# Kernel optimization log

Hardware: AMD Instinct MI355X
Metric: run time of the kernel (lower is better)

## Reference

```python
import jax, jax.numpy as jnp
import numpy as np

B, C, W, H = 4, 128, 64, 64
CK = 32  # f/g projection channels


def setup_inputs() -> dict:
    key = jax.random.key(0)
    ks = jax.random.split(key, 8)
    s_in = 1.0 / np.sqrt(C)
    return {
        "x": jax.random.normal(ks[0], (B, C, W, H), dtype=jnp.float32),
        "Wf": jax.random.normal(ks[1], (CK, C), dtype=jnp.float32) * s_in,
        "bf": jnp.zeros((CK,), dtype=jnp.float32),
        "Wg": jax.random.normal(ks[2], (CK, C), dtype=jnp.float32) * s_in,
        "bg": jnp.zeros((CK,), dtype=jnp.float32),
        "Wh": jax.random.normal(ks[3], (C, C), dtype=jnp.float32) * s_in,
        "bh": jnp.zeros((C,), dtype=jnp.float32),
        "gamma": jax.random.normal(ks[4], (1,), dtype=jnp.float32) * 0.1,
    }


def reference(x, Wf, bf, Wg, bg, Wh, bh, gamma):
    b, c, w, h = x.shape
    n = w * h
    xf = x.reshape(b, c, n)                                  # [B,C,N]
    # 1x1 convs == per-pixel linear projections
    f = jnp.einsum('oc,bcn->bon', Wf, xf) + bf[None, :, None]  # [B,32,N]
    g = jnp.einsum('oc,bcn->bon', Wg, xf) + bg[None, :, None]  # [B,32,N]
    v = jnp.einsum('oc,bcn->bon', Wh, xf) + bh[None, :, None]  # [B,C,N]
    # attention = softmax(f^T g) over last dim (g positions), as in the torch code
    att = jax.nn.softmax(jnp.einsum('bkn,bkm->bnm', f, g), axis=-1)  # [B,N,N]
    # self_attention = h @ attention  (contract over f-position axis)
    sa = jnp.einsum('bcn,bnm->bcm', v, att).reshape(b, c, w, h)
    return gamma[0] * sa + x
```

## Files before the change

kernel.cpp:

```cpp
#include <hip/hip_runtime.h>
#include <hip/hip_bf16.h>

#define BB 4
#define CC 128
#define NN 4096
#define CK 32
#define L2E 1.442695040888963f

typedef __attribute__((ext_vector_type(8))) short short8v;
typedef __attribute__((ext_vector_type(4))) float float4v;

__device__ inline ushort f2bf(float f) {
    union { __hip_bfloat16 h; ushort u; } cv;
    cv.h = __float2bfloat16(f);
    return cv.u;
}
__device__ inline uint pk2(float lo, float hi) {
    return ((uint)f2bf(lo)) | ((uint)f2bf(hi) << 16);
}
__device__ __forceinline__ void gll16(const void* g, void* l) {
    __builtin_amdgcn_global_load_lds(
        (const __attribute__((address_space(1))) void*)g,
        (__attribute__((address_space(3))) void*)l, 16, 0, 0);
}
__device__ __forceinline__ void gll4(const void* g, void* l) {
    __builtin_amdgcn_global_load_lds(
        (const __attribute__((address_space(1))) void*)g,
        (__attribute__((address_space(3))) void*)l, 4, 0, 0);
}

__global__ __launch_bounds__(1024) void proj_kernel(
    const float* __restrict__ x,
    const float* __restrict__ Wf, const float* __restrict__ bf,
    const float* __restrict__ Wg, const float* __restrict__ bg,
    const float* __restrict__ Wh, const float* __restrict__ bh,
    const float* __restrict__ gamma,
    ushort* __restrict__ ft, ushort* __restrict__ gt, ushort* __restrict__ vh)
{
    __shared__ float xs[CC][64];
    const int t  = threadIdx.x;
    const int n0 = blockIdx.x * 64;
    const int b  = blockIdx.y;
    const float* xb = x + (size_t)b * CC * NN + n0;

    {
        const int j  = t & 63;
        const int cb = t >> 6;
        #pragma unroll
        for (int i = 0; i < 8; ++i)
            xs[cb + 16 * i][j] = xb[(size_t)(cb + 16 * i) * NN + j];
    }
    __syncthreads();

    const int jq = t & 15;
    const int og = (t >> 4) & 15;
    const int i3 = t >> 8;

    const float* wrow[3];
    float biasv[3];
    int   mode[3], oc[3];
    #pragma unroll
    for (int ii = 0; ii < 3; ++ii) {
        const int i = i3 * 3 + ii;
        if (i < 2)      { oc[ii] = og + 16 * i;       wrow[ii] = Wf + oc[ii] * CC; biasv[ii] = bf[oc[ii]]; mode[ii] = 0; }
        else if (i < 4) { oc[ii] = og + 16 * (i - 2); wrow[ii] = Wg + oc[ii] * CC; biasv[ii] = bg[oc[ii]]; mode[ii] = 1; }
        else            { oc[ii] = og + 16 * (i - 4); wrow[ii] = Wh + oc[ii] * CC; biasv[ii] = bh[oc[ii]]; mode[ii] = 2; }
    }

    float acc[3][4];
    #pragma unroll
    for (int ii = 0; ii < 3; ++ii)
        #pragma unroll
        for (int jj = 0; jj < 4; ++jj) acc[ii][jj] = 0.f;

    #pragma unroll 4
    for (int c4 = 0; c4 < 32; ++c4) {
        float4 wv[3];
        #pragma unroll
        for (int ii = 0; ii < 3; ++ii)
            wv[ii] = *reinterpret_cast<const float4*>(&wrow[ii][c4 * 4]);
        #pragma unroll
        for (int q = 0; q < 4; ++q) {
            const float4 xv = *reinterpret_cast<const float4*>(&xs[c4 * 4 + q][jq * 4]);
            #pragma unroll
            for (int ii = 0; ii < 3; ++ii) {
                const float wq = (q == 0) ? wv[ii].x : (q == 1) ? wv[ii].y
                               : (q == 2) ? wv[ii].z : wv[ii].w;
                acc[ii][0] += wq * xv.x;
                acc[ii][1] += wq * xv.y;
                acc[ii][2] += wq * xv.z;
                acc[ii][3] += wq * xv.w;
            }
        }
    }

    const float sgn = (gamma[0] < 0.f) ? -1.f : 1.f;
    const int n_base = n0 + jq * 4;
    #pragma unroll
    for (int ii = 0; ii < 3; ++ii) {
        if (mode[ii] == 0) {
            #pragma unroll
            for (int jj = 0; jj < 4; ++jj)
                ft[((size_t)b * NN + n_base + jj) * CK + oc[ii]] = f2bf(acc[ii][jj] + biasv[ii]);
        } else if (mode[ii] == 1) {
            #pragma unroll
            for (int jj = 0; jj < 4; ++jj)
                gt[((size_t)b * NN + n_base + jj) * CK + oc[ii]] = f2bf(acc[ii][jj] + biasv[ii]);
        } else {
            ushort4 pkv;
            pkv.x = f2bf(sgn * (acc[ii][0] + biasv[ii]));
            pkv.y = f2bf(sgn * (acc[ii][1] + biasv[ii]));
            pkv.z = f2bf(sgn * (acc[ii][2] + biasv[ii]));
            pkv.w = f2bf(sgn * (acc[ii][3] + biasv[ii]));
            *reinterpret_cast<ushort4*>(&vh[((size_t)b * CC + oc[ii]) * NN + n_base]) = pkv;
        }
    }
}

__global__ __launch_bounds__(256) void pass1_kernel(
    const ushort* __restrict__ ft, const ushort* __restrict__ gt,
    float* __restrict__ Dpart)
{
    const int t   = threadIdx.x;
    const int w   = t >> 6;
    const int l   = t & 63;
    const int g16 = l >> 4;
    const int l16 = l & 15;
    const int n0  = blockIdx.x * 64;
    const int b   = blockIdx.y;
    const int mz  = blockIdx.z;

    const ushort* ftb = ft + (size_t)b * NN * CK;
    const ushort* gtb = gt + (size_t)b * NN * CK;

    const short8v afrag = *reinterpret_cast<const short8v*>(
        &ftb[(size_t)(n0 + 16 * w + l16) * CK + 8 * g16]);

    const float4v zf = {0.f, 0.f, 0.f, 0.f};
    float d0 = 0.f, d1 = 0.f, d2 = 0.f, d3 = 0.f;
    const int m0 = mz * 512;

    short8v bfA = *reinterpret_cast<const short8v*>(
        &gtb[(size_t)(m0 + l16) * CK + 8 * g16]);
    #pragma unroll 1
    for (int mt = 0; mt < 32; mt += 2) {
        const short8v bfB = *reinterpret_cast<const short8v*>(
            &gtb[(size_t)(m0 + (mt + 1) * 16 + l16) * CK + 8 * g16]);
        float4v s = __builtin_amdgcn_mfma_f32_16x16x32_bf16(afrag, bfA, zf, 0, 0, 0);
        d0 += __expf(s[0]); d1 += __expf(s[1]); d2 += __expf(s[2]); d3 += __expf(s[3]);
        bfA = *reinterpret_cast<const short8v*>(
            &gtb[(size_t)(m0 + (((mt + 2) & 31)) * 16 + l16) * CK + 8 * g16]);
        float4v s2 = __builtin_amdgcn_mfma_f32_16x16x32_bf16(afrag, bfB, zf, 0, 0, 0);
        d0 += __expf(s2[0]); d1 += __expf(s2[1]); d2 += __expf(s2[2]); d3 += __expf(s2[3]);
    }
    #pragma unroll
    for (int msk = 1; msk <= 8; msk <<= 1) {
        d0 += __shfl_xor(d0, msk);
        d1 += __shfl_xor(d1, msk);
        d2 += __shfl_xor(d2, msk);
        d3 += __shfl_xor(d3, msk);
    }
    if (l16 < 4) {
        const int n = n0 + 16 * w + 4 * g16 + l16;
        const float v = (l16 == 0) ? d0 : (l16 == 1) ? d1 : (l16 == 2) ? d2 : d3;
        Dpart[((size_t)b * NN + n) * 8 + mz] = v;
    }
}

__global__ __launch_bounds__(256) void reduce_kernel(
    const float* __restrict__ Dpart, float* __restrict__ Ld,
    const float* __restrict__ gamma)
{
    const int i = blockIdx.x * 256 + threadIdx.x;
    const float4 a4 = *reinterpret_cast<const float4*>(&Dpart[(size_t)i * 8]);
    const float4 b4 = *reinterpret_cast<const float4*>(&Dpart[(size_t)i * 8 + 4]);
    const float D = (a4.x + a4.y + a4.z + a4.w) + (b4.x + b4.y + b4.z + b4.w);
    Ld[i] = log2f(fabsf(gamma[0])) - log2f(D);
}

#define V_OFF 0
#define F_OFF 4096
#define L_OFF 6144
#define BUFB  6400
#define WSTR  12800

__global__ __launch_bounds__(512) void pass2_kernel(
    const ushort* __restrict__ ft, const ushort* __restrict__ gt,
    const ushort* __restrict__ vh, const float* __restrict__ Ld,
    const float* __restrict__ x, float* __restrict__ out)
{
    __shared__ __align__(16) char smem[8 * WSTR];

    const int t   = threadIdx.x;
    const int w   = t >> 6;
    const int l   = t & 63;
    const int g16 = l >> 4;
    const int l16 = l & 15;
    const int ch  = w & 1;
    const int nq  = w >> 1;

    const int bid = blockIdx.x;
    const int xcd = bid & 7;
    const int b   = xcd >> 1;
    const int m0  = ((bid >> 3) + 32 * (xcd & 1)) * 64;

    const ushort* ftb = ft + (size_t)b * NN * CK;
    const ushort* gtb = gt + (size_t)b * NN * CK;
    const ushort* vhb = vh + (size_t)b * CC * NN;
    const float*  ldb = Ld + (size_t)b * NN;

    char* wsm = smem + w * WSTR;

    short8v gfrag[4];
    #pragma unroll
    for (int tm = 0; tm < 4; ++tm)
        gfrag[tm] = *reinterpret_cast<const short8v*>(
            &gtb[(size_t)(m0 + 16 * tm + l16) * CK + 8 * g16]);

    const float4v zf = {0.f, 0.f, 0.f, 0.f};
    float4v acc[4][4];
    #pragma unroll
    for (int tc = 0; tc < 4; ++tc)
        #pragma unroll
        for (int tm = 0; tm < 4; ++tm) acc[tc][tm] = zf;

    const int nbase = nq * 1024;
    const int rr = l >> 2, cp = l & 3;

#define STAGE(n0_, bo_) do {                                                   \
    _Pragma("unroll")                                                          \
    for (int j = 0; j < 4; ++j) {                                              \
        const int row = j * 16 + rr;                                           \
        gll16(vhb + (size_t)(64 * ch + row) * NN + (n0_)                       \
                  + (((2 * cp) ^ (row & 6)) << 2),                             \
              wsm + (bo_) + V_OFF + j * 1024);                                 \
    }                                                                          \
    _Pragma("unroll")                                                          \
    for (int j = 0; j < 2; ++j) {                                              \
        const int row = j * 16 + rr;                                           \
        gll16(ftb + (size_t)((n0_) + row) * CK + cp * 8,                       \
              wsm + (bo_) + F_OFF + j * 1024);                                 \
    }                                                                          \
    gll4(ldb + (n0_) + (l & 31), wsm + (bo_) + L_OFF);                         \
} while (0)

    STAGE(nbase, 0);
    asm volatile("s_waitcnt vmcnt(0)" ::: "memory");

    int bo = 0;
    #pragma unroll 1
    for (int st = 0; st < 32; ++st) {
        const int n0 = nbase + st * 32;
        if (st < 31) {
            STAGE(n0 + 32, bo ^ BUFB);
            asm volatile("s_waitcnt vmcnt(7)" ::: "memory");
        } else {
            asm volatile("s_waitcnt vmcnt(0)" ::: "memory");
        }

        const char*  Vb = wsm + bo + V_OFF;
        const char*  Fb = wsm + bo + F_OFF;
        const float* Lb = (const float*)(wsm + bo + L_OFF);

        const short8v af0 = *reinterpret_cast<const short8v*>(Fb + l16 * 64 + g16 * 16);
        const short8v af1 = *reinterpret_cast<const short8v*>(Fb + (16 + l16) * 64 + g16 * 16);
        const float4  ld0 = *reinterpret_cast<const float4*>(Lb + 4 * g16);
        const float4  ld1 = *reinterpret_cast<const float4*>(Lb + 16 + 4 * g16);

        union { uint u[4]; short8v s; } pf[4];
        #pragma unroll
        for (int tm = 0; tm < 4; ++tm) {
            float4v s0 = __builtin_amdgcn_mfma_f32_16x16x32_bf16(af0, gfrag[tm], zf, 0, 0, 0);
            float4v s1 = __builtin_amdgcn_mfma_f32_16x16x32_bf16(af1, gfrag[tm], zf, 0, 0, 0);
            pf[tm].u[0] = pk2(__builtin_amdgcn_exp2f(fmaf(s0[0], L2E, ld0.x)),
                              __builtin_amdgcn_exp2f(fmaf(s0[1], L2E, ld0.y)));
            pf[tm].u[1] = pk2(__builtin_amdgcn_exp2f(fmaf(s0[2], L2E, ld0.z)),
                              __builtin_amdgcn_exp2f(fmaf(s0[3], L2E, ld0.w)));
            pf[tm].u[2] = pk2(__builtin_amdgcn_exp2f(fmaf(s1[0], L2E, ld1.x)),
                              __builtin_amdgcn_exp2f(fmaf(s1[1], L2E, ld1.y)));
            pf[tm].u[3] = pk2(__builtin_amdgcn_exp2f(fmaf(s1[2], L2E, ld1.z)),
                              __builtin_amdgcn_exp2f(fmaf(s1[3], L2E, ld1.w)));
        }

        #pragma unroll
        for (int tc = 0; tc < 4; ++tc) {
            const int cl = 16 * tc + l16;
            const uint2 va = *reinterpret_cast<const uint2*>(
                Vb + cl * 64 + 8 * (g16 ^ (cl & 6)));
            const uint2 vb2 = *reinterpret_cast<const uint2*>(
                Vb + cl * 64 + 8 * ((4 + g16) ^ (cl & 6)));
            union { uint u[4]; short8v s; } av;
            av.u[0] = va.x;  av.u[1] = va.y;
            av.u[2] = vb2.x; av.u[3] = vb2.y;
            #pragma unroll
            for (int tm = 0; tm < 4; ++tm)
                acc[tc][tm] = __builtin_amdgcn_mfma_f32_16x16x32_bf16(av.s, pf[tm].s, acc[tc][tm], 0, 0, 0);
        }
        bo ^= BUFB;
    }
#undef STAGE

    __syncthreads();
    float4v* rl = (float4v*)smem;
    if (nq != 0) {
        const int slot = (nq - 1) * 2 + ch;
        #pragma unroll
        for (int tc = 0; tc < 4; ++tc)
            #pragma unroll
            for (int tm = 0; tm < 4; ++tm)
                rl[(slot * 16 + tc * 4 + tm) * 64 + l] = acc[tc][tm];
    }
    __syncthreads();
    if (nq == 0) {
        const float* xb = x   + (size_t)b * CC * NN;
        float*       ob = out + (size_t)b * CC * NN;
        #pragma unroll
        for (int tc = 0; tc < 4; ++tc) {
            #pragma unroll
            for (int tm = 0; tm < 4; ++tm) {
                const int fi = tc * 4 + tm;
                float4v s = acc[tc][tm]
                          + rl[((ch) * 16 + fi) * 64 + l]
                          + rl[((2 + ch) * 16 + fi) * 64 + l]
                          + rl[((4 + ch) * 16 + fi) * 64 + l];
                const int cb = 64 * ch + 16 * tc + 4 * g16;
                const int m  = m0 + 16 * tm + l16;
                #pragma unroll
                for (int r = 0; r < 4; ++r) {
                    const size_t idx = (size_t)(cb + r) * NN + m;
                    ob[idx] = s[r] + xb[idx];
                }
            }
        }
    }
}

extern "C" void kernel_launch(void* const* d_in, const int* in_sizes, int n_in,
                              void* d_out, int out_size, void* d_ws, size_t ws_size,
                              hipStream_t stream)
{
    const float* x     = (const float*)d_in[0];
    const float* Wf    = (const float*)d_in[1];
    const float* bf    = (const float*)d_in[2];
    const float* Wg    = (const float*)d_in[3];
    const float* bg    = (const float*)d_in[4];
    const float* Wh    = (const float*)d_in[5];
    const float* bh    = (const float*)d_in[6];
    const float* gamma = (const float*)d_in[7];

    ushort* ft = (ushort*)d_ws;
    ushort* gt = ft + (size_t)BB * NN * CK;
    ushort* vh = gt + (size_t)BB * NN * CK;
    float* Dpart = (float*)(vh + (size_t)BB * CC * NN);
    float* Ld    = Dpart + (size_t)BB * NN * 8;

    float* out = (float*)d_out;

    proj_kernel<<<dim3(NN / 64, BB), 1024, 0, stream>>>(x, Wf, bf, Wg, bg, Wh, bh, gamma, ft, gt, vh);
    pass1_kernel<<<dim3(NN / 64, BB, 8), 256, 0, stream>>>(ft, gt, Dpart);
    reduce_kernel<<<dim3(BB * NN / 256), 256, 0, stream>>>(Dpart, Ld, gamma);
    pass2_kernel<<<dim3(256), 512, 0, stream>>>(ft, gt, vh, Ld, x, out);
}
```

Baseline: 87.15 us.

## Fold softmax normalization into V and log2e into f, restructure pass2 tiling

```diff
diff --git a/kernel.cpp b/kernel.cpp
--- a/kernel.cpp
+++ b/kernel.cpp
@@ -15,6 +15,11 @@
     cv.h = __float2bfloat16(f);
     return cv.u;
 }
+__device__ inline float bf2f(ushort u) {
+    union { uint u; float f; } cv;
+    cv.u = ((uint)u) << 16;
+    return cv.f;
+}
 __device__ inline uint pk2(float lo, float hi) {
     return ((uint)f2bf(lo)) | ((uint)f2bf(hi) << 16);
 }
@@ -22,11 +27,6 @@
     __builtin_amdgcn_global_load_lds(
         (const __attribute__((address_space(1))) void*)g,
         (__attribute__((address_space(3))) void*)l, 16, 0, 0);
-}
-__device__ __forceinline__ void gll4(const void* g, void* l) {
-    __builtin_amdgcn_global_load_lds(
-        (const __attribute__((address_space(1))) void*)g,
-        (__attribute__((address_space(3))) void*)l, 4, 0, 0);
 }
 
 __global__ __launch_bounds__(1024) void proj_kernel(
@@ -101,7 +101,8 @@
         if (mode[ii] == 0) {
             #pragma unroll
             for (int jj = 0; jj < 4; ++jj)
-                ft[((size_t)b * NN + n_base + jj) * CK + oc[ii]] = f2bf(acc[ii][jj] + biasv[ii]);
+                ft[((size_t)b * NN + n_base + jj) * CK + oc[ii]] =
+                    f2bf((acc[ii][jj] + biasv[ii]) * L2E);
         } else if (mode[ii] == 1) {
             #pragma unroll
             for (int jj = 0; jj < 4; ++jj)
@@ -147,11 +148,13 @@
         const short8v bfB = *reinterpret_cast<const short8v*>(
             &gtb[(size_t)(m0 + (mt + 1) * 16 + l16) * CK + 8 * g16]);
         float4v s = __builtin_amdgcn_mfma_f32_16x16x32_bf16(afrag, bfA, zf, 0, 0, 0);
-        d0 += __expf(s[0]); d1 += __expf(s[1]); d2 += __expf(s[2]); d3 += __expf(s[3]);
+        d0 += __builtin_amdgcn_exp2f(s[0]); d1 += __builtin_amdgcn_exp2f(s[1]);
+        d2 += __builtin_amdgcn_exp2f(s[2]); d3 += __builtin_amdgcn_exp2f(s[3]);
         bfA = *reinterpret_cast<const short8v*>(
             &gtb[(size_t)(m0 + (((mt + 2) & 31)) * 16 + l16) * CK + 8 * g16]);
         float4v s2 = __builtin_amdgcn_mfma_f32_16x16x32_bf16(afrag, bfB, zf, 0, 0, 0);
-        d0 += __expf(s2[0]); d1 += __expf(s2[1]); d2 += __expf(s2[2]); d3 += __expf(s2[3]);
+        d0 += __builtin_amdgcn_exp2f(s2[0]); d1 += __builtin_amdgcn_exp2f(s2[1]);
+        d2 += __builtin_amdgcn_exp2f(s2[2]); d3 += __builtin_amdgcn_exp2f(s2[3]);
     }
     #pragma unroll
     for (int msk = 1; msk <= 8; msk <<= 1) {
@@ -168,25 +171,48 @@
 }
 
 __global__ __launch_bounds__(256) void reduce_kernel(
-    const float* __restrict__ Dpart, float* __restrict__ Ld,
+    const float* __restrict__ Dpart, float* __restrict__ sc,
     const float* __restrict__ gamma)
 {
     const int i = blockIdx.x * 256 + threadIdx.x;
     const float4 a4 = *reinterpret_cast<const float4*>(&Dpart[(size_t)i * 8]);
     const float4 b4 = *reinterpret_cast<const float4*>(&Dpart[(size_t)i * 8 + 4]);
     const float D = (a4.x + a4.y + a4.z + a4.w) + (b4.x + b4.y + b4.z + b4.w);
-    Ld[i] = log2f(fabsf(gamma[0])) - log2f(D);
-}
-
-#define V_OFF 0
-#define F_OFF 4096
-#define L_OFF 6144
-#define BUFB  6400
-#define WSTR  12800
+    sc[i] = fabsf(gamma[0]) / D;
+}
+
+__global__ __launch_bounds__(256) void vscale_kernel(
+    ushort* __restrict__ vh, const float* __restrict__ sc)
+{
+    const size_t i8   = (size_t)blockIdx.x * 256 + threadIdx.x;
+    const size_t base = i8 * 8;
+    const int    n    = (int)(base & (NN - 1));
+    const int    b    = (int)(base / ((size_t)CC * NN));
+
+    ushort4 v0 = *reinterpret_cast<const ushort4*>(&vh[base]);
+    ushort4 v1 = *reinterpret_cast<const ushort4*>(&vh[base + 4]);
+    const float4 s0 = *reinterpret_cast<const float4*>(&sc[(size_t)b * NN + n]);
+    const float4 s1 = *reinterpret_cast<const float4*>(&sc[(size_t)b * NN + n + 4]);
+
+    v0.x = f2bf(bf2f(v0.x) * s0.x);
+    v0.y = f2bf(bf2f(v0.y) * s0.y);
+    v0.z = f2bf(bf2f(v0.z) * s0.z);
+    v0.w = f2bf(bf2f(v0.w) * s0.w);
+    v1.x = f2bf(bf2f(v1.x) * s1.x);
+    v1.y = f2bf(bf2f(v1.y) * s1.y);
+    v1.z = f2bf(bf2f(v1.z) * s1.z);
+    v1.w = f2bf(bf2f(v1.w) * s1.w);
+
+    *reinterpret_cast<ushort4*>(&vh[base])     = v0;
+    *reinterpret_cast<ushort4*>(&vh[base + 4]) = v1;
+}
+
+#define WSTR  16384
+#define VBUF  8192
 
 __global__ __launch_bounds__(512) void pass2_kernel(
     const ushort* __restrict__ ft, const ushort* __restrict__ gt,
-    const ushort* __restrict__ vh, const float* __restrict__ Ld,
+    const ushort* __restrict__ vh,
     const float* __restrict__ x, float* __restrict__ out)
 {
     __shared__ __align__(16) char smem[8 * WSTR];
@@ -196,7 +222,7 @@
     const int l   = t & 63;
     const int g16 = l >> 4;
     const int l16 = l & 15;
-    const int ch  = w & 1;
+    const int mq  = w & 1;
     const int nq  = w >> 1;
 
     const int bid = blockIdx.x;
@@ -207,41 +233,33 @@
     const ushort* ftb = ft + (size_t)b * NN * CK;
     const ushort* gtb = gt + (size_t)b * NN * CK;
     const ushort* vhb = vh + (size_t)b * CC * NN;
-    const float*  ldb = Ld + (size_t)b * NN;
 
     char* wsm = smem + w * WSTR;
 
-    short8v gfrag[4];
-    #pragma unroll
-    for (int tm = 0; tm < 4; ++tm)
+    short8v gfrag[2];
+    #pragma unroll
+    for (int tm = 0; tm < 2; ++tm)
         gfrag[tm] = *reinterpret_cast<const short8v*>(
-            &gtb[(size_t)(m0 + 16 * tm + l16) * CK + 8 * g16]);
+            &gtb[(size_t)(m0 + 32 * mq + 16 * tm + l16) * CK + 8 * g16]);
 
     const float4v zf = {0.f, 0.f, 0.f, 0.f};
-    float4v acc[4][4];
-    #pragma unroll
-    for (int tc = 0; tc < 4; ++tc)
-        #pragma unroll
-        for (int tm = 0; tm < 4; ++tm) acc[tc][tm] = zf;
+    float4v acc[8][2];
+    #pragma unroll
+    for (int tc = 0; tc < 8; ++tc)
+        #pragma unroll
+        for (int tm = 0; tm < 2; ++tm) acc[tc][tm] = zf;
 
     const int nbase = nq * 1024;
     const int rr = l >> 2, cp = l & 3;
 
 #define STAGE(n0_, bo_) do {                                                   \
     _Pragma("unroll")                                                          \
-    for (int j = 0; j < 4; ++j) {                                              \
+    for (int j = 0; j < 8; ++j) {                                              \
         const int row = j * 16 + rr;                                           \
-        gll16(vhb + (size_t)(64 * ch + row) * NN + (n0_)                       \
+        gll16(vhb + (size_t)row * NN + (n0_)                                   \
                   + (((2 * cp) ^ (row & 6)) << 2),                             \
-              wsm + (bo_) + V_OFF + j * 1024);                                 \
+              wsm + (bo_) + j * 1024);                                         \
     }                                                                          \
-    _Pragma("unroll")                                                          \
-    for (int j = 0; j < 2; ++j) {                                              \
-        const int row = j * 16 + rr;                                           \
-        gll16(ftb + (size_t)((n0_) + row) * CK + cp * 8,                       \
-              wsm + (bo_) + F_OFF + j * 1024);                                 \
-    }                                                                          \
-    gll4(ldb + (n0_) + (l & 31), wsm + (bo_) + L_OFF);                         \
 } while (0)
 
     STAGE(nbase, 0);
@@ -251,80 +269,74 @@
     #pragma unroll 1
     for (int st = 0; st < 32; ++st) {
         const int n0 = nbase + st * 32;
+
+        const short8v af0 = *reinterpret_cast<const short8v*>(
+            &ftb[(size_t)(n0 + l16) * CK + 8 * g16]);
+        const short8v af1 = *reinterpret_cast<const short8v*>(
+            &ftb[(size_t)(n0 + 16 + l16) * CK + 8 * g16]);
+
         if (st < 31) {
-            STAGE(n0 + 32, bo ^ BUFB);
-            asm volatile("s_waitcnt vmcnt(7)" ::: "memory");
+            STAGE(n0 + 32, bo ^ VBUF);
+            asm volatile("s_waitcnt vmcnt(8)" ::: "memory");
         } else {
             asm volatile("s_waitcnt vmcnt(0)" ::: "memory");
         }
 
-        const char*  Vb = wsm + bo + V_OFF;
-        const char*  Fb = wsm + bo + F_OFF;
-        const float* Lb = (const float*)(wsm + bo + L_OFF);
-
-        const short8v af0 = *reinterpret_cast<const short8v*>(Fb + l16 * 64 + g16 * 16);
-        const short8v af1 = *reinterpret_cast<const short8v*>(Fb + (16 + l16) * 64 + g16 * 16);
-        const float4  ld0 = *reinterpret_cast<const float4*>(Lb + 4 * g16);
-        const float4  ld1 = *reinterpret_cast<const float4*>(Lb + 16 + 4 * g16);
-
-        union { uint u[4]; short8v s; } pf[4];
-        #pragma unroll
-        for (int tm = 0; tm < 4; ++tm) {
+        const char* Vb = wsm + bo;
+
+        union { uint u[4]; short8v s; } pf[2];
+        #pragma unroll
+        for (int tm = 0; tm < 2; ++tm) {
             float4v s0 = __builtin_amdgcn_mfma_f32_16x16x32_bf16(af0, gfrag[tm], zf, 0, 0, 0);
             float4v s1 = __builtin_amdgcn_mfma_f32_16x16x32_bf16(af1, gfrag[tm], zf, 0, 0, 0);
-            pf[tm].u[0] = pk2(__builtin_amdgcn_exp2f(fmaf(s0[0], L2E, ld0.x)),
-                              __builtin_amdgcn_exp2f(fmaf(s0[1], L2E, ld0.y)));
-            pf[tm].u[1] = pk2(__builtin_amdgcn_exp2f(fmaf(s0[2], L2E, ld0.z)),
-                              __builtin_amdgcn_exp2f(fmaf(s0[3], L2E, ld0.w)));
-            pf[tm].u[2] = pk2(__builtin_amdgcn_exp2f(fmaf(s1[0], L2E, ld1.x)),
-                              __builtin_amdgcn_exp2f(fmaf(s1[1], L2E, ld1.y)));
-            pf[tm].u[3] = pk2(__builtin_amdgcn_exp2f(fmaf(s1[2], L2E, ld1.z)),
-                              __builtin_amdgcn_exp2f(fmaf(s1[3], L2E, ld1.w)));
-        }
-
-        #pragma unroll
-        for (int tc = 0; tc < 4; ++tc) {
+            pf[tm].u[0] = pk2(__builtin_amdgcn_exp2f(s0[0]), __builtin_amdgcn_exp2f(s0[1]));
+            pf[tm].u[1] = pk2(__builtin_amdgcn_exp2f(s0[2]), __builtin_amdgcn_exp2f(s0[3]));
+            pf[tm].u[2] = pk2(__builtin_amdgcn_exp2f(s1[0]), __builtin_amdgcn_exp2f(s1[1]));
+            pf[tm].u[3] = pk2(__builtin_amdgcn_exp2f(s1[2]), __builtin_amdgcn_exp2f(s1[3]));
+        }
+
+        #pragma unroll
+        for (int tc = 0; tc < 8; ++tc) {
             const int cl = 16 * tc + l16;
-            const uint2 va = *reinterpret_cast<const uint2*>(
+            const uint2 va  = *reinterpret_cast<const uint2*>(
                 Vb + cl * 64 + 8 * (g16 ^ (cl & 6)));
             const uint2 vb2 = *reinterpret_cast<const uint2*>(
                 Vb + cl * 64 + 8 * ((4 + g16) ^ (cl & 6)));
             union { uint u[4]; short8v s; } av;
             av.u[0] = va.x;  av.u[1] = va.y;
             av.u[2] = vb2.x; av.u[3] = vb2.y;
-            #pragma unroll
-            for (int tm = 0; tm < 4; ++tm)
-                acc[tc][tm] = __builtin_amdgcn_mfma_f32_16x16x32_bf16(av.s, pf[tm].s, acc[tc][tm], 0, 0, 0);
-        }
-        bo ^= BUFB;
+            acc[tc][0] = __builtin_amdgcn_mfma_f32_16x16x32_bf16(av.s, pf[0].s, acc[tc][0], 0, 0, 0);
+            acc[tc][1] = __builtin_amdgcn_mfma_f32_16x16x32_bf16(av.s, pf[1].s, acc[tc][1], 0, 0, 0);
+        }
+        bo ^= VBUF;
     }
 #undef STAGE
 
     __syncthreads();
     float4v* rl = (float4v*)smem;
     if (nq != 0) {
-        const int slot = (nq - 1) * 2 + ch;
-        #pragma unroll
-        for (int tc = 0; tc < 4; ++tc)
-            #pragma unroll
-            for (int tm = 0; tm < 4; ++tm)
-                rl[(slot * 16 + tc * 4 + tm) * 64 + l] = acc[tc][tm];
+        const int slot = (nq - 1) * 2 + mq;
+        #pragma unroll
+        for (int tc = 0; tc < 8; ++tc)
+            #pragma unroll
+            for (int tm = 0; tm < 2; ++tm)
+                rl[(slot * 16 + tc * 2 + tm) * 64 + l] = acc[tc][tm];
     }
     __syncthreads();
     if (nq == 0) {
         const float* xb = x   + (size_t)b * CC * NN;
         float*       ob = out + (size_t)b * CC * NN;
         #pragma unroll
-        for (int tc = 0; tc < 4; ++tc) {
-            #pragma unroll
-            for (int tm = 0; tm < 4; ++tm) {
-                const int fi = tc * 4 + tm;
+        for (int tc = 0; tc < 8; ++tc) {
+            #pragma unroll
+            for (int tm = 0; tm < 2; ++tm) {
+                const int fi = tc * 2 + tm;
                 float4v s = acc[tc][tm]
-                          + rl[((ch) * 16 + fi) * 64 + l]
-                          + rl[((2 + ch) * 16 + fi) * 64 + l]
-                          + rl[((4 + ch) * 16 + fi) * 64 + l];
-                const int cb = 64 * ch + 16 * tc + 4 * g16;
-                const int m  = m0 + 16 * tm + l16;
+                          + rl[((mq) * 16 + fi) * 64 + l]
+                          + rl[((2 + mq) * 16 + fi) * 64 + l]
+                          + rl[((4 + mq) * 16 + fi) * 64 + l];
+                const int cb = 16 * tc + 4 * g16;
+                const int m  = m0 + 32 * mq + 16 * tm + l16;
                 #pragma unroll
                 for (int r = 0; r < 4; ++r) {
                     const size_t idx = (size_t)(cb + r) * NN + m;
@@ -352,12 +364,13 @@
     ushort* gt = ft + (size_t)BB * NN * CK;
     ushort* vh = gt + (size_t)BB * NN * CK;
     float* Dpart = (float*)(vh + (size_t)BB * CC * NN);
-    float* Ld    = Dpart + (size_t)BB * NN * 8;
+    float* sc    = Dpart + (size_t)BB * NN * 8;
 
     float* out = (float*)d_out;
 
     proj_kernel<<<dim3(NN / 64, BB), 1024, 0, stream>>>(x, Wf, bf, Wg, bg, Wh, bh, gamma, ft, gt, vh);
     pass1_kernel<<<dim3(NN / 64, BB, 8), 256, 0, stream>>>(ft, gt, Dpart);
-    reduce_kernel<<<dim3(BB * NN / 256), 256, 0, stream>>>(Dpart, Ld, gamma);
-    pass2_kernel<<<dim3(256), 512, 0, stream>>>(ft, gt, vh, Ld, x, out);
-}
+    reduce_kernel<<<dim3(BB * NN / 256), 256, 0, stream>>>(Dpart, sc, gamma);
+    vscale_kernel<<<dim3(BB * CC * NN / 8 / 256), 256, 0, stream>>>(vh, sc);
+    pass2_kernel<<<dim3(256), 512, 0, stream>>>(ft, gt, vh, x, out);
+}
```

After: 83.53 us. 4.2% less time.
